# Optimization experiments

Hardware: AMD Instinct MI355X
Metric: run time of the kernel (lower is better)

## Reference

```python
import jax, jax.numpy as jnp
import numpy as np

B, QL, KL, D, H = 2, 512, 8192, 1024, 8
HD = D // H  # head dim = 128


def setup_inputs() -> dict:
    key = jax.random.key(0)
    ks = jax.random.split(key, 12)
    s = 0.02
    return {
        "inputs_q": jax.random.normal(ks[0], (B, QL, D), jnp.float32),
        "inputs_k": jax.random.normal(ks[1], (B, KL, D), jnp.float32),
        "inputs_v": jax.random.normal(ks[2], (B, KL, D), jnp.float32),
        "attention_mask": jax.random.randint(ks[3], (B, QL, KL), 0, 2).astype(bool),
        "Wq": jax.random.normal(ks[4], (D, D), jnp.float32) * s,
        "bq": jnp.zeros((D,), jnp.float32),
        "Wk": jax.random.normal(ks[5], (D, D), jnp.float32) * s,
        "bk": jnp.zeros((D,), jnp.float32),
        "Wv": jax.random.normal(ks[6], (D, D), jnp.float32) * s,
        "bv": jnp.zeros((D,), jnp.float32),
        "Wf": jax.random.normal(ks[7], (D, D), jnp.float32) * s,
        "bf": jnp.zeros((D,), jnp.float32),
    }


def reference(inputs_q, inputs_k, inputs_v, attention_mask, Wq, bq, Wk, bk, Wv, bv, Wf, bf):
    # Projections (torch Linear: x @ W.T + b)
    q = inputs_q @ Wq.T + bq  # [B, QL, D]
    k = inputs_k @ Wk.T + bk  # [B, KL, D]
    v = inputs_v @ Wv.T + bv  # [B, KL, D]

    q = q.reshape(B, QL, H, HD)
    k = k.reshape(B, KL, H, HD)
    v = v.reshape(B, KL, H, HD)

    # scores [B, H, QL, KL]
    scores = jnp.einsum("bqhd,bkhd->bhqk", q, k)
    scale = 1.0 / np.sqrt(HD).astype(np.float32)
    scores = scores * scale
    large_k = jnp.float32(1e30)
    scores = jnp.where(attention_mask[:, None, :, :], scores, -large_k)

    probs = jax.nn.softmax(scores, axis=-1)
    # note: original calls self.dropout(normalized) but discards the result -> no-op

    summed = jnp.einsum("bhqk,bkhd->bqhd", probs, v).reshape(B, QL, H * HD)

    # wipe rows whose mask is all zero
    wipe = jnp.all(~attention_mask, axis=2, keepdims=True)  # [B, QL, 1]
    summed = jnp.where(wipe, jnp.zeros_like(summed), summed)

    return summed @ Wf.T + bf
```

## Files before the change

kernel.cpp:

```cpp
#include <hip/hip_runtime.h>
#include <hip/hip_bf16.h>
#include <math.h>

typedef __attribute__((ext_vector_type(4))) float fx4;
typedef __attribute__((ext_vector_type(4))) short sx4;
typedef __attribute__((ext_vector_type(8))) short sx8;
typedef unsigned long long u64;

#define MFMA16(a, b, c) __builtin_amdgcn_mfma_f32_16x16x16bf16_1k(a, b, c, 0, 0, 0)
#define MFMA32(a, b, c) __builtin_amdgcn_mfma_f32_16x16x32_bf16(a, b, c, 0, 0, 0)

__device__ __forceinline__ unsigned short f2bf(float f) {
  unsigned int u = __float_as_uint(f);
  return (unsigned short)((u + 0x7fffu + ((u >> 16) & 1u)) >> 16);
}

__device__ __forceinline__ unsigned cvtpk(float lo, float hi) {
  unsigned r;
  asm("v_cvt_pk_bf16_f32 %0, %1, %2" : "=v"(r) : "v"(lo), "v"(hi));
  return r;
}

typedef const __attribute__((address_space(1))) char* gc1p;
typedef __attribute__((address_space(3))) char* lc3p;
__device__ __forceinline__ void glds16(const void* g, const void* lds_uniform) {
  gc1p gp = (gc1p)(unsigned long long)(uintptr_t)g;
  lc3p lp = (lc3p)(unsigned)__builtin_amdgcn_readfirstlane((int)(unsigned)(uintptr_t)lds_uniform);
  __builtin_amdgcn_global_load_lds(gp, lp, 16, 0, 0);
}

__global__ __launch_bounds__(256) void k_prep(
    const float* __restrict__ Wq, const float* __restrict__ Wk,
    const float* __restrict__ Wv, const float* __restrict__ Wf,
    const int* __restrict__ mask, short* cwq, short* cwk, short* cwv,
    short* cwf, u64* __restrict__ mb) {
  __shared__ unsigned char nib[256];
  const int bx = blockIdx.x;
  const int t = threadIdx.x;
  if (bx >= 2048) {
    const int mbx = bx - 2048;
    const int4 m = *(const int4*)(mask + (size_t)mbx * 1024 + t * 4);
    nib[t] = (unsigned char)((m.x != 0) | ((m.y != 0) << 1) | ((m.z != 0) << 2) |
                             ((m.w != 0) << 3));
    __syncthreads();
    if (t < 16) {
      u64 wv = 0;
#pragma unroll
      for (int i = 0; i < 16; i++) wv |= (u64)(nib[t * 16 + i] & 0xF) << (4 * i);
      mb[(size_t)mbx * 16 + t] = wv;
    }
    return;
  }
  const int seg = bx >> 9;
  const float* s = seg == 0 ? Wq : seg == 1 ? Wk : seg == 2 ? Wv : Wf;
  short* d = seg == 0 ? cwq : seg == 1 ? cwk : seg == 2 ? cwv : cwf;
  size_t i = (size_t)(bx & 511) * 2048 + (size_t)t * 8;
  const fx4 a = *(const fx4*)(s + i);
  const fx4 b = *(const fx4*)(s + i + 4);
  sx8 o;
  o[0] = (short)f2bf(a[0]); o[1] = (short)f2bf(a[1]);
  o[2] = (short)f2bf(a[2]); o[3] = (short)f2bf(a[3]);
  o[4] = (short)f2bf(b[0]); o[5] = (short)f2bf(b[1]);
  o[6] = (short)f2bf(b[2]); o[7] = (short)f2bf(b[3]);
  *(sx8*)(d + i) = o;
}

template <int MODE, int MT, int AF32>
__device__ __forceinline__ void gemm_body(short* sA, short* sB,
                                          const void* __restrict__ Aptr,
                                          const short* __restrict__ Bw,
                                          const float* __restrict__ bias,
                                          void* __restrict__ Cptr, int M, int N,
                                          int K, float alpha, int bx) {
  const int t = threadIdx.x;
  const int lane = t & 63;
  const int w = t >> 6;
  const int quad = lane >> 4;
  const int l16 = lane & 15;
  const int x7 = l16 & 7;
  int m0, n0;
  if (M >= 8192) {
    const int ml = bx & 7, nn = (bx >> 3) & 7, mh = bx >> 6;
    m0 = (mh * 8 + ml) * MT;
    n0 = nn << 7;
  } else {
    const int ntile = N >> 7;
    n0 = (bx % ntile) << 7;
    m0 = (bx / ntile) * MT;
  }
  constexpr int NI = (MT == 128) ? 4 : 2;
  constexpr int NJ = (MT == 128) ? 4 : 2;
  const int wm = (MT == 128) ? ((w >> 1) << 6) : 0;
  const int wn = (MT == 128) ? ((w & 1) << 6) : (w << 5);
  const fx4 fzero = {0.f, 0.f, 0.f, 0.f};
  fx4 acc[4][NI];
#pragma unroll
  for (int i = 0; i < 4; i++)
#pragma unroll
    for (int j = 0; j < NI; j++) acc[i][j] = fzero;

  const int srow = lane >> 3;
  const int scb = lane & 7;

  for (int k0 = 0; k0 < K; k0 += 64) {
    fx4 ra[NJ][2];
    if (AF32) {
      const float* Af = (const float*)Aptr;
#pragma unroll
      for (int j = 0; j < NJ; j++) {
        const int rbase = (MT == 128) ? (w * 32 + j * 8) : (j * 32 + w * 8);
        const int row = rbase + srow;
        const int cb = scb ^ (row & 7);
        const float* src = Af + (size_t)(m0 + row) * K + k0 + cb * 8;
        ra[j][0] = *(const fx4*)src;
        ra[j][1] = *(const fx4*)(src + 4);
      }
    }
    __syncthreads();
    if (!AF32) {
      const short* A = (const short*)Aptr;
#pragma unroll
      for (int j = 0; j < NJ; j++) {
        const int rbase = (MT == 128) ? (w * 32 + j * 8) : (j * 32 + w * 8);
        const int row = rbase + srow;
        const int cb = scb ^ (row & 7);
        glds16(A + (size_t)(m0 + row) * K + k0 + cb * 8, &sA[rbase * 64]);
      }
    }
#pragma unroll
    for (int j = 0; j < 4; j++) {
      const int row = w * 32 + j * 8 + srow;
      const int cb = scb ^ (row & 7);
      glds16(Bw + (size_t)(n0 + row) * K + k0 + cb * 8, &sB[(w * 32 + j * 8) * 64]);
    }
    if (AF32) {
#pragma unroll
      for (int j = 0; j < NJ; j++) {
        const int rbase = (MT == 128) ? (w * 32 + j * 8) : (j * 32 + w * 8);
        sx8 o;
        unsigned* ou = (unsigned*)&o;
        ou[0] = cvtpk(ra[j][0][0], ra[j][0][1]);
        ou[1] = cvtpk(ra[j][0][2], ra[j][0][3]);
        ou[2] = cvtpk(ra[j][1][0], ra[j][1][1]);
        ou[3] = cvtpk(ra[j][1][2], ra[j][1][3]);
        *(sx8*)(&sA[rbase * 64 + lane * 8]) = o;
      }
    }
    __syncthreads();
#pragma unroll
    for (int kc = 0; kc < 2; kc++) {
      const int cbp = ((kc * 4 + quad) ^ x7) * 8;
      sx8 fa[4], fb[NI];
#pragma unroll
      for (int i = 0; i < 4; i++)
        fa[i] = *(const sx8*)(&sA[(wm + i * 16 + l16) * 64 + cbp]);
#pragma unroll
      for (int i = 0; i < NI; i++)
        fb[i] = *(const sx8*)(&sB[(wn + i * 16 + l16) * 64 + cbp]);
#pragma unroll
      for (int mi = 0; mi < 4; mi++)
#pragma unroll
        for (int ni = 0; ni < NI; ni++)
          acc[mi][ni] = MFMA32(fa[mi], fb[ni], acc[mi][ni]);
    }
  }
#pragma unroll
  for (int ni = 0; ni < NI; ni++) {
    const int col = n0 + wn + ni * 16 + l16;
    const float bval = bias[col];
    if (MODE == 2) {
#pragma unroll
      for (int mi = 0; mi < 4; mi++) {
        const int rowb = m0 + wm + mi * 16 + quad * 4;
        const int bb = rowb >> 13;
        const int kl = (rowb & 8191) ^ ((col & 8) ? 4 : 0);
        sx4 pkv;
#pragma unroll
        for (int r = 0; r < 4; r++) pkv[r] = (short)f2bf(acc[mi][ni][r] + bval);
        *(sx4*)((unsigned short*)Cptr + ((size_t)bb * 1024 + col) * 8192 + kl) = pkv;
      }
    } else {
#pragma unroll
      for (int mi = 0; mi < 4; mi++)
#pragma unroll
        for (int r = 0; r < 4; r++) {
          const int row = m0 + wm + mi * 16 + quad * 4 + r;
          const float v = (acc[mi][ni][r] + bval) * alpha;
          if (MODE == 1) ((float*)Cptr)[(size_t)row * N + col] = v;
          else ((unsigned short*)Cptr)[(size_t)row * N + col] = f2bf(v);
        }
    }
  }
}

__global__ __launch_bounds__(256) void k_gemm_k(const float* __restrict__ ink,
                                                const short* __restrict__ cwk,
                                                const float* __restrict__ bk,
                                                short* __restrict__ Kp) {
  __shared__ __align__(16) short smem[16384];
  gemm_body<0, 128, 1>(smem, smem + 8192, ink, cwk, bk, Kp, 16384, 1024, 1024,
                       1.f, blockIdx.x);
}

__global__ __launch_bounds__(256) void k_proj_vq(
    const float* __restrict__ inv, const short* __restrict__ cwv,
    const float* __restrict__ bv, short* __restrict__ Vt,
    const float* __restrict__ inq, const short* __restrict__ cwq,
    const float* __restrict__ bq, short* __restrict__ Qp, float alpha_q) {
  __shared__ __align__(16) short smem[16384];
  const int bx = blockIdx.x;
  if (bx < 128)
    gemm_body<0, 64, 1>(smem, smem + 8192, inq, cwq, bq, Qp, 1024, 1024, 1024,
                        alpha_q, bx);
  else
    gemm_body<2, 128, 1>(smem, smem + 8192, inv, cwv, bv, Vt, 16384, 1024, 1024,
                         1.f, bx - 128);
}

__global__ __launch_bounds__(256) void k_gemm_out(const short* __restrict__ summed,
                                                  const short* __restrict__ cwf,
                                                  const float* __restrict__ bf,
                                                  float* __restrict__ out) {
  __shared__ __align__(16) short smem[16384];
  gemm_body<1, 64, 0>(smem, smem + 8192, summed, cwf, bf, out, 1024, 1024, 1024,
                      1.f, blockIdx.x);
}

__global__ __launch_bounds__(256, 4) void k_attn(const short* __restrict__ Qp,
                                                 const short* __restrict__ Kp,
                                                 const short* __restrict__ Vt,
                                                 const u64* __restrict__ mb,
                                                 float* __restrict__ ml,
                                                 float* __restrict__ Op) {
  __shared__ __align__(16) short sK[8192];
  __shared__ __align__(16) short sV[8192];
  const int x = blockIdx.x;
  const int gl = x & 7;
  const int qt = (x >> 3) & 7;
  const int gh = x >> 6;
  const int g = gh * 8 + gl;
  const int s = g & 7;
  const int h = (g >> 3) & 7;
  const int b = g >> 6;
  const int li = ((b * 8 + h) * 8 + qt) * 8 + s;
  const int t = threadIdx.x;
  const int lane = t & 63;
  const int w = t >> 6;
  const int quad = lane >> 4;
  const int l16 = lane & 15;
  const int x7 = l16 & 7;
  const int q0 = qt << 6;
  const fx4 fzero = {0.f, 0.f, 0.f, 0.f};

  const short* qbase = Qp + (size_t)(b * 512 + q0 + w * 16 + l16) * 1024 + h * 128;
  sx8 aq[4];
#pragma unroll
  for (int kc = 0; kc < 4; kc++) aq[kc] = *(const sx8*)(qbase + kc * 32 + quad * 8);

  fx4 Ot[8];
#pragma unroll
  for (int d = 0; d < 8; d++) Ot[d] = fzero;
  float lsum = 0.f;

  const short* kbase = Kp + (size_t)(b * 8192 + s * 1024) * 1024 + h * 128;
  const short* vbase = Vt + (size_t)(b * 1024 + h * 128) * 8192 + s * 1024;
  const u64* wdp = mb + (size_t)(b * 512 + q0 + w * 16 + l16) * 128 + s * 16;
  const int srow4 = lane >> 4, scb16 = lane & 15;
  const int srow8 = lane >> 3, scb8 = lane & 7;
  const int h4 = ((quad & 1) ^ ((l16 >> 3) & 1)) * 4;

  for (int kt = 0; kt < 16; kt++) {
    __syncthreads();
#pragma unroll
    for (int j = 0; j < 4; j++) {
      const int row = (w * 4 + j) * 4 + srow4;
      const int cb = scb16 ^ (row & 7);
      glds16(kbase + (size_t)(kt * 64 + row) * 1024 + cb * 8, &sK[(w * 4 + j) * 512]);
    }
#pragma unroll
    for (int j = 0; j < 4; j++) {
      const int row = (w * 4 + j) * 8 + srow8;
      const int cb = scb8 ^ (row & 7);
      glds16(vbase + (size_t)row * 8192 + kt * 64 + cb * 8, &sV[(w * 4 + j) * 512]);
    }
    const u64 wd = wdp[kt];
    __syncthreads();
    const unsigned lo = (unsigned)wd, hi = (unsigned)(wd >> 32);
    sx4 pk[4];
#pragma unroll
    for (int nt = 0; nt < 4; nt++) {
      fx4 a = fzero;
#pragma unroll
      for (int kc = 0; kc < 4; kc++) {
        const sx8 kf = *(const sx8*)(&sK[(nt * 16 + l16) * 128 + ((kc * 4 + quad) ^ x7) * 8]);
        a = MFMA32(kf, aq[kc], a);
      }
      const unsigned bits = (nt & 2) ? hi : lo;
      const int sh = (nt & 1) * 16 + quad * 4;
      float pv[4];
#pragma unroll
      for (int r = 0; r < 4; r++) {
        const float e = __builtin_amdgcn_exp2f(a[r]);
        pv[r] = ((bits >> (sh + r)) & 1u) ? e : 0.f;
        lsum += pv[r];
      }
      sx4 pko;
      ((unsigned*)&pko)[0] = __builtin_amdgcn_perm(
          __float_as_uint(pv[1]) + 0x8000u, __float_as_uint(pv[0]) + 0x8000u, 0x07060302u);
      ((unsigned*)&pko)[1] = __builtin_amdgcn_perm(
          __float_as_uint(pv[3]) + 0x8000u, __float_as_uint(pv[2]) + 0x8000u, 0x07060302u);
      pk[nt] = pko;
    }
#pragma unroll
    for (int dt = 0; dt < 8; dt++) {
      fx4 o = Ot[dt];
#pragma unroll
      for (int nt = 0; nt < 4; nt++) {
        const int cb = (2 * nt + (quad >> 1)) ^ x7;
        const sx4 vf = *(const sx4*)(&sV[(dt * 16 + l16) * 64 + cb * 8 + h4]);
        o = MFMA16(vf, pk[nt], o);
      }
      Ot[dt] = o;
    }
  }
  lsum += __shfl_xor(lsum, 16, 64);
  lsum += __shfl_xor(lsum, 32, 64);
  if (lane < 16) ml[(size_t)li * 64 + w * 16 + l16] = lsum;
  float* ob = Op + (size_t)li * 8192 + (w * 16 + l16) * 128 + quad * 4;
#pragma unroll
  for (int dt = 0; dt < 8; dt++) *(fx4*)(ob + dt * 16) = Ot[dt];
}

__global__ __launch_bounds__(256) void k_combine(const float* __restrict__ ml,
                                                 const float* __restrict__ Op,
                                                 short* __restrict__ summed) {
  const int xc = blockIdx.x;
  const int qt = xc & 7;
  const int h = (xc >> 3) & 7;
  const int b = xc >> 6;
  const int t = threadIdx.x;
  const int row = t >> 2;
  const int dg = (t & 3) * 32;
  float L = 0.f;
#pragma unroll
  for (int s = 0; s < 8; s++) L += ml[(size_t)(xc * 8 + s) * 64 + row];
  float o[32];
#pragma unroll
  for (int i = 0; i < 32; i++) o[i] = 0.f;
  if (L != 0.f) {
#pragma unroll
    for (int s = 0; s < 8; s++) {
      const float* src = Op + (size_t)(xc * 8 + s) * 8192 + row * 128 + dg;
#pragma unroll
      for (int i = 0; i < 8; i++) {
        const fx4 v = *(const fx4*)(src + i * 4);
        o[i * 4 + 0] += v[0]; o[i * 4 + 1] += v[1];
        o[i * 4 + 2] += v[2]; o[i * 4 + 3] += v[3];
      }
    }
    const float inv = 1.f / L;
#pragma unroll
    for (int i = 0; i < 32; i++) o[i] *= inv;
  }
  short* dst = summed + (size_t)(b * 512 + qt * 64 + row) * 1024 + h * 128 + dg;
#pragma unroll
  for (int i = 0; i < 4; i++) {
    sx8 pkv;
#pragma unroll
    for (int j = 0; j < 8; j++) pkv[j] = (short)f2bf(o[i * 8 + j]);
    *(sx8*)(dst + i * 8) = pkv;
  }
}

extern "C" void kernel_launch(void* const* d_in, const int* in_sizes, int n_in,
                              void* d_out, int out_size, void* d_ws, size_t ws_size,
                              hipStream_t stream) {
  (void)in_sizes; (void)n_in; (void)out_size; (void)ws_size;
  const float* inq = (const float*)d_in[0];
  const float* ink = (const float*)d_in[1];
  const float* inv = (const float*)d_in[2];
  const int* mask = (const int*)d_in[3];
  const float* Wq = (const float*)d_in[4];
  const float* bq = (const float*)d_in[5];
  const float* Wk = (const float*)d_in[6];
  const float* bk = (const float*)d_in[7];
  const float* Wv = (const float*)d_in[8];
  const float* bv = (const float*)d_in[9];
  const float* Wf = (const float*)d_in[10];
  const float* bf = (const float*)d_in[11];

  char* ws = (char*)d_ws;
  short* Vt = (short*)(ws + 0);
  short* Kp = (short*)(ws + 33554432);
  float* Op = (float*)(ws + 67108864);
  short* cwq = (short*)(ws + 102760448);
  short* cwk = (short*)(ws + 104857600);
  short* cwv = (short*)(ws + 106954752);
  short* cwf = (short*)(ws + 109051904);
  short* Qp = (short*)(ws + 111149056);
  short* summed = (short*)(ws + 113246208);
  u64* mb = (u64*)(ws + 115343360);
  float* ml = (float*)(ws + 116391936);

  const float alpha_q = 0.12751757f;

  k_prep<<<10240, 256, 0, stream>>>(Wq, Wk, Wv, Wf, mask, cwq, cwk, cwv, cwf, mb);
  k_gemm_k<<<1024, 256, 0, stream>>>(ink, cwk, bk, Kp);
  k_proj_vq<<<1152, 256, 0, stream>>>(inv, cwv, bv, Vt, inq, cwq, bq, Qp, alpha_q);
  k_attn<<<1024, 256, 0, stream>>>(Qp, Kp, Vt, mb, ml, Op);
  k_combine<<<128, 256, 0, stream>>>(ml, Op, summed);
  k_gemm_out<<<128, 256, 0, stream>>>(summed, cwf, bf, (float*)d_out);
}
```

Measured before the change: 405.2 us.

## Prefetch fp32 A tiles across K loop, coarsen prep blocks, split combine

The fp32-A GEMM path now loads the next K-slice of A into registers right after the LDS barrier, so those global loads overlap the MFMA work of the current slice instead of stalling at the top of each iteration. The prep kernel handles four mask rows and four times as many weight elements per block, cutting the grid from 10240 to 2304 blocks. The combine kernel splits each tile across two blocks over the head dimension, doubling its grid to 256 for more parallelism. The prefetch raises register pressure in the GEMM kernels, which could lower occupancy.

```diff
diff --git a/kernel.cpp b/kernel.cpp
--- a/kernel.cpp
+++ b/kernel.cpp
@@ -34,35 +34,51 @@
     const float* __restrict__ Wv, const float* __restrict__ Wf,
     const int* __restrict__ mask, short* cwq, short* cwk, short* cwv,
     short* cwf, u64* __restrict__ mb) {
-  __shared__ unsigned char nib[256];
+  __shared__ unsigned char nib[4][256];
   const int bx = blockIdx.x;
   const int t = threadIdx.x;
-  if (bx >= 2048) {
-    const int mbx = bx - 2048;
-    const int4 m = *(const int4*)(mask + (size_t)mbx * 1024 + t * 4);
-    nib[t] = (unsigned char)((m.x != 0) | ((m.y != 0) << 1) | ((m.z != 0) << 2) |
-                             ((m.w != 0) << 3));
+  if (bx >= 256) {
+    const int mrow0 = (bx - 256) * 4;
+#pragma unroll
+    for (int j = 0; j < 4; j++) {
+      const int4 m = *(const int4*)(mask + (size_t)(mrow0 + j) * 1024 + t * 4);
+      nib[j][t] = (unsigned char)((m.x != 0) | ((m.y != 0) << 1) |
+                                  ((m.z != 0) << 2) | ((m.w != 0) << 3));
+    }
     __syncthreads();
-    if (t < 16) {
+    if (t < 64) {
+      const int j = t >> 4, i = t & 15;
       u64 wv = 0;
 #pragma unroll
-      for (int i = 0; i < 16; i++) wv |= (u64)(nib[t * 16 + i] & 0xF) << (4 * i);
-      mb[(size_t)mbx * 16 + t] = wv;
+      for (int k = 0; k < 16; k++)
+        wv |= (u64)(nib[j][i * 16 + k] & 0xF) << (4 * k);
+      mb[(size_t)(mrow0 + j) * 16 + i] = wv;
     }
     return;
   }
-  const int seg = bx >> 9;
+  const int seg = bx >> 6;
   const float* s = seg == 0 ? Wq : seg == 1 ? Wk : seg == 2 ? Wv : Wf;
   short* d = seg == 0 ? cwq : seg == 1 ? cwk : seg == 2 ? cwv : cwf;
-  size_t i = (size_t)(bx & 511) * 2048 + (size_t)t * 8;
-  const fx4 a = *(const fx4*)(s + i);
-  const fx4 b = *(const fx4*)(s + i + 4);
-  sx8 o;
-  o[0] = (short)f2bf(a[0]); o[1] = (short)f2bf(a[1]);
-  o[2] = (short)f2bf(a[2]); o[3] = (short)f2bf(a[3]);
-  o[4] = (short)f2bf(b[0]); o[5] = (short)f2bf(b[1]);
-  o[6] = (short)f2bf(b[2]); o[7] = (short)f2bf(b[3]);
-  *(sx8*)(d + i) = o;
+  const size_t base = (size_t)(bx & 63) * 16384;
+#pragma unroll
+  for (int it = 0; it < 4; it++) {
+    const size_t i = base + (size_t)it * 4096 + (size_t)t * 16;
+    const fx4 a0 = *(const fx4*)(s + i);
+    const fx4 a1 = *(const fx4*)(s + i + 4);
+    const fx4 a2 = *(const fx4*)(s + i + 8);
+    const fx4 a3 = *(const fx4*)(s + i + 12);
+    sx8 o0, o1;
+    o0[0] = (short)f2bf(a0[0]); o0[1] = (short)f2bf(a0[1]);
+    o0[2] = (short)f2bf(a0[2]); o0[3] = (short)f2bf(a0[3]);
+    o0[4] = (short)f2bf(a1[0]); o0[5] = (short)f2bf(a1[1]);
+    o0[6] = (short)f2bf(a1[2]); o0[7] = (short)f2bf(a1[3]);
+    o1[0] = (short)f2bf(a2[0]); o1[1] = (short)f2bf(a2[1]);
+    o1[2] = (short)f2bf(a2[2]); o1[3] = (short)f2bf(a2[3]);
+    o1[4] = (short)f2bf(a3[0]); o1[5] = (short)f2bf(a3[1]);
+    o1[6] = (short)f2bf(a3[2]); o1[7] = (short)f2bf(a3[3]);
+    *(sx8*)(d + i) = o0;
+    *(sx8*)(d + i + 8) = o1;
+  }
 }
 
 template <int MODE, int MT, int AF32>
@@ -101,38 +117,24 @@
 
   const int srow = lane >> 3;
   const int scb = lane & 7;
+  const float* Af = (const float*)Aptr;
+  const short* Ab = (const short*)Aptr;
+  fx4 ra[NJ][2];
+
+  if (AF32) {
+#pragma unroll
+    for (int j = 0; j < NJ; j++) {
+      const int rbase = (MT == 128) ? (w * 32 + j * 8) : (j * 32 + w * 8);
+      const int row = rbase + srow;
+      const int cb = scb ^ (row & 7);
+      const float* src = Af + (size_t)(m0 + row) * K + cb * 8;
+      ra[j][0] = *(const fx4*)src;
+      ra[j][1] = *(const fx4*)(src + 4);
+    }
+  }
 
   for (int k0 = 0; k0 < K; k0 += 64) {
-    fx4 ra[NJ][2];
-    if (AF32) {
-      const float* Af = (const float*)Aptr;
-#pragma unroll
-      for (int j = 0; j < NJ; j++) {
-        const int rbase = (MT == 128) ? (w * 32 + j * 8) : (j * 32 + w * 8);
-        const int row = rbase + srow;
-        const int cb = scb ^ (row & 7);
-        const float* src = Af + (size_t)(m0 + row) * K + k0 + cb * 8;
-        ra[j][0] = *(const fx4*)src;
-        ra[j][1] = *(const fx4*)(src + 4);
-      }
-    }
     __syncthreads();
-    if (!AF32) {
-      const short* A = (const short*)Aptr;
-#pragma unroll
-      for (int j = 0; j < NJ; j++) {
-        const int rbase = (MT == 128) ? (w * 32 + j * 8) : (j * 32 + w * 8);
-        const int row = rbase + srow;
-        const int cb = scb ^ (row & 7);
-        glds16(A + (size_t)(m0 + row) * K + k0 + cb * 8, &sA[rbase * 64]);
-      }
-    }
-#pragma unroll
-    for (int j = 0; j < 4; j++) {
-      const int row = w * 32 + j * 8 + srow;
-      const int cb = scb ^ (row & 7);
-      glds16(Bw + (size_t)(n0 + row) * K + k0 + cb * 8, &sB[(w * 32 + j * 8) * 64]);
-    }
     if (AF32) {
 #pragma unroll
       for (int j = 0; j < NJ; j++) {
@@ -145,8 +147,33 @@
         ou[3] = cvtpk(ra[j][1][2], ra[j][1][3]);
         *(sx8*)(&sA[rbase * 64 + lane * 8]) = o;
       }
+    } else {
+#pragma unroll
+      for (int j = 0; j < NJ; j++) {
+        const int rbase = (MT == 128) ? (w * 32 + j * 8) : (j * 32 + w * 8);
+        const int row = rbase + srow;
+        const int cb = scb ^ (row & 7);
+        glds16(Ab + (size_t)(m0 + row) * K + k0 + cb * 8, &sA[rbase * 64]);
+      }
+    }
+#pragma unroll
+    for (int j = 0; j < 4; j++) {
+      const int row = w * 32 + j * 8 + srow;
+      const int cb = scb ^ (row & 7);
+      glds16(Bw + (size_t)(n0 + row) * K + k0 + cb * 8, &sB[(w * 32 + j * 8) * 64]);
     }
     __syncthreads();
+    if (AF32 && k0 + 64 < K) {
+#pragma unroll
+      for (int j = 0; j < NJ; j++) {
+        const int rbase = (MT == 128) ? (w * 32 + j * 8) : (j * 32 + w * 8);
+        const int row = rbase + srow;
+        const int cb = scb ^ (row & 7);
+        const float* src = Af + (size_t)(m0 + row) * K + (k0 + 64) + cb * 8;
+        ra[j][0] = *(const fx4*)src;
+        ra[j][1] = *(const fx4*)(src + 4);
+      }
+    }
 #pragma unroll
     for (int kc = 0; kc < 2; kc++) {
       const int cbp = ((kc * 4 + quad) ^ x7) * 8;
@@ -334,25 +361,27 @@
 __global__ __launch_bounds__(256) void k_combine(const float* __restrict__ ml,
                                                  const float* __restrict__ Op,
                                                  short* __restrict__ summed) {
-  const int xc = blockIdx.x;
+  const int bx = blockIdx.x;
+  const int xc = bx >> 1;
+  const int dh = (bx & 1) * 64;
   const int qt = xc & 7;
   const int h = (xc >> 3) & 7;
   const int b = xc >> 6;
   const int t = threadIdx.x;
   const int row = t >> 2;
-  const int dg = (t & 3) * 32;
+  const int dg = dh + (t & 3) * 16;
   float L = 0.f;
 #pragma unroll
   for (int s = 0; s < 8; s++) L += ml[(size_t)(xc * 8 + s) * 64 + row];
-  float o[32];
-#pragma unroll
-  for (int i = 0; i < 32; i++) o[i] = 0.f;
+  float o[16];
+#pragma unroll
+  for (int i = 0; i < 16; i++) o[i] = 0.f;
   if (L != 0.f) {
 #pragma unroll
     for (int s = 0; s < 8; s++) {
       const float* src = Op + (size_t)(xc * 8 + s) * 8192 + row * 128 + dg;
 #pragma unroll
-      for (int i = 0; i < 8; i++) {
+      for (int i = 0; i < 4; i++) {
         const fx4 v = *(const fx4*)(src + i * 4);
         o[i * 4 + 0] += v[0]; o[i * 4 + 1] += v[1];
         o[i * 4 + 2] += v[2]; o[i * 4 + 3] += v[3];
@@ -360,11 +389,11 @@
     }
     const float inv = 1.f / L;
 #pragma unroll
-    for (int i = 0; i < 32; i++) o[i] *= inv;
+    for (int i = 0; i < 16; i++) o[i] *= inv;
   }
   short* dst = summed + (size_t)(b * 512 + qt * 64 + row) * 1024 + h * 128 + dg;
 #pragma unroll
-  for (int i = 0; i < 4; i++) {
+  for (int i = 0; i < 2; i++) {
     sx8 pkv;
 #pragma unroll
     for (int j = 0; j < 8; j++) pkv[j] = (short)f2bf(o[i * 8 + j]);
@@ -404,10 +433,10 @@
 
   const float alpha_q = 0.12751757f;
 
-  k_prep<<<10240, 256, 0, stream>>>(Wq, Wk, Wv, Wf, mask, cwq, cwk, cwv, cwf, mb);
+  k_prep<<<2304, 256, 0, stream>>>(Wq, Wk, Wv, Wf, mask, cwq, cwk, cwv, cwf, mb);
   k_gemm_k<<<1024, 256, 0, stream>>>(ink, cwk, bk, Kp);
   k_proj_vq<<<1152, 256, 0, stream>>>(inv, cwv, bv, Vt, inq, cwq, bq, Qp, alpha_q);
   k_attn<<<1024, 256, 0, stream>>>(Qp, Kp, Vt, mb, ml, Op);
-  k_combine<<<128, 256, 0, stream>>>(ml, Op, summed);
+  k_combine<<<256, 256, 0, stream>>>(ml, Op, summed);
   k_gemm_out<<<128, 256, 0, stream>>>(summed, cwf, bf, (float*)d_out);
 }
```

After: 387.1 us. 1.05x faster.
